# Kernel optimization log

Measured on AMD Instinct MI355X. Metric: run time of the kernel, lower is better.

Reference implementation:

```python
import jax, jax.numpy as jnp
import numpy as np
from jax import lax

GAMMA = 1.0  # init gamma


def setup_inputs() -> dict:
    key = jax.random.key(0)
    k = jax.random.split(key, 6)
    B, T1, T2, D, WD = 64, 320, 320, 768, 32
    x = jax.random.normal(k[0], (B, T1, D), jnp.float32)
    y = jax.random.normal(k[1], (B, T2, D), jnp.float32)
    # nn.Linear(input_dim, warp_dim): weight [WD, D], bias [WD]
    W = jax.random.normal(k[2], (WD, D), jnp.float32) / np.sqrt(D).astype(np.float32)
    b = 0.01 * jax.random.normal(k[3], (WD,), jnp.float32)
    warp_scale = 1.0 + 0.1 * jax.random.normal(k[4], (WD,), jnp.float32)
    warp_shift = 0.1 * jax.random.normal(k[5], (WD,), jnp.float32)
    return {"x": x, "y": y, "W": W, "b": b, "warp_scale": warp_scale, "warp_shift": warp_shift}


def _soft_dtw_path(xw, yw, gamma):
    # Faithful banded soft-DTW DP: cells outside the band stay 0 and ARE read
    # by in-band neighbors, exactly as the torch loop does.
    B, T1, _ = xw.shape
    T2 = yw.shape[1]
    bw = max(T1, T2) // 4 + 1
    # squared euclidean distances [B,T1,T2] (expanded form to avoid B*T1*T2*D blow-up)
    x2 = jnp.sum(xw * xw, -1)[:, :, None]
    y2 = jnp.sum(yw * yw, -1)[:, None, :]
    dist = x2 + y2 - 2.0 * jnp.einsum('bid,bjd->bij', xw, yw)
    NEG = jnp.float32(-1e30)  # disables a candidate inside logsumexp
    t2s = jnp.arange(T2)

    def outer(prev_row, xs):  # prev_row: path[t1-1, :] of shape [B,T2]
        t1, drow = xs  # drow: dist[:, t1, :] -> [B,T2]
        diag_prev = jnp.concatenate([jnp.zeros((B, 1), drow.dtype), prev_row[:, :-1]], axis=1)

        def inner(left, ins):  # left: path[t1, t2-1] -> [B]
            t2, d, up, diag = ins
            z = jnp.stack([
                jnp.where((t1 > 0) & (t2 > 0), -diag / gamma, NEG),
                jnp.where(t1 > 0, -up / gamma, NEG),
                jnp.where(t2 > 0, -left / gamma, NEG),
            ], axis=0)  # [3,B]
            softmin = -gamma * jax.nn.logsumexp(z, axis=0)
            val = d + jnp.where((t1 > 0) | (t2 > 0), softmin, 0.0)
            in_band = (t2 >= t1 - bw) & (t2 <= t1 + bw - 1)
            val = jnp.where(in_band, val, 0.0)
            return val, val

        _, row = lax.scan(inner, jnp.zeros((B,), drow.dtype),
                          (t2s, drow.T, prev_row.T, diag_prev.T))
        row = row.T  # [B,T2]
        return row, row

    _, path = lax.scan(outer, jnp.zeros((B, T2), dist.dtype),
                       (jnp.arange(T1), jnp.transpose(dist, (1, 0, 2))))
    path = jnp.transpose(path, (1, 0, 2))  # [B,T1,T2]
    return jax.nn.softmax(-path / gamma, axis=-1)


def reference(x, y, W, b, warp_scale, warp_shift):
    xw = (x @ W.T + b) * warp_scale + warp_shift
    yw = (y @ W.T + b) * warp_scale + warp_shift
    path = _soft_dtw_path(xw, yw, GAMMA)  # [B,T1,T2] softmax probs
    pn = path / (jnp.sum(path, axis=1, keepdims=True) + 1e-10)
    aligned = jnp.einsum('bts,btd->bsd', pn, x)  # bmm(path^T, x) -> [B,T2,D]
    return aligned, path
```

## Files before the change

### kernel.cpp

```cpp
#include <hip/hip_runtime.h>

#define NB 64
#define T 320
#define D 768
#define WD 32
#define NSTEP 639
#define NBLK 80
#define BSTRIDE (NBLK * 1024)
#define BIG 1e30f
#define LOG2E 1.44269504088896340736f
#define LN2 0.69314718055994530942f

__device__ __forceinline__ float dpp_ror1(float v) {
  return __int_as_float(__builtin_amdgcn_update_dpp(
      0, __float_as_int(v), 0x13C, 0xF, 0xF, true));
}
__device__ __forceinline__ float dpp_rol1(float v) {
  return __int_as_float(__builtin_amdgcn_update_dpp(
      0, __float_as_int(v), 0x134, 0xF, 0xF, true));
}

__global__ __launch_bounds__(256) void prep_kernel(
    const float* __restrict__ W, const float* __restrict__ bias,
    const float* __restrict__ wscale, const float* __restrict__ wshift,
    float* __restrict__ WeT, float* __restrict__ beff) {
  int i = blockIdx.x * 256 + threadIdx.x;
  int c = i >> 5, k = i & 31;
  WeT[i] = W[k * D + c] * wscale[k];
  if (i < WD) beff[i] = bias[i] * wscale[i] + wshift[i];
}

__global__ __launch_bounds__(256) void proj_kernel(
    const float* __restrict__ x, const float* __restrict__ y,
    const float* __restrict__ WeT, const float* __restrict__ beff,
    float* __restrict__ xw, float* __restrict__ yw) {
  __shared__ float lds[8448];
  int tid = threadIdx.x;
  int w = tid >> 6, l = tid & 63;
  int rbase = blockIdx.x * 64;
  float acc[32];
#pragma unroll
  for (int k = 0; k < 32; ++k) acc[k] = 0.f;
#pragma clang loop unroll(disable)
  for (int ch = 0; ch < 6; ++ch) {
    __syncthreads();
#pragma unroll
    for (int p = 0; p < 8; ++p) {
      int idx = p * 256 + tid;
      int row = idx >> 5;
      int c4 = idx & 31;
      int r = rbase + row;
      const float* src = (r < NB * T) ? x + (size_t)r * D
                                      : y + (size_t)(r - NB * T) * D;
      float4 v = *(const float4*)(src + ch * 128 + c4 * 4);
      lds[row * 129 + c4 * 4 + 0] = v.x;
      lds[row * 129 + c4 * 4 + 1] = v.y;
      lds[row * 129 + c4 * 4 + 2] = v.z;
      lds[row * 129 + c4 * 4 + 3] = v.w;
    }
    __syncthreads();
    int woff = __builtin_amdgcn_readfirstlane((ch * 128 + w * 32) * 32);
    const float* wp = WeT + woff;
#pragma unroll
    for (int cc = 0; cc < 32; ++cc) {
      float xv = lds[l * 129 + w * 32 + cc];
#pragma unroll
      for (int k = 0; k < 32; ++k)
        acc[k] = fmaf(wp[cc * 32 + k], xv, acc[k]);
    }
  }
  __syncthreads();
#pragma unroll
  for (int k = 0; k < 32; ++k) lds[w * 2112 + l * 33 + k] = acc[k];
  __syncthreads();
  int idx = tid * 8;
  int row = idx >> 5;
  int k0 = idx & 31;
  float o[8];
#pragma unroll
  for (int e = 0; e < 8; ++e)
    o[e] = lds[0 * 2112 + row * 33 + k0 + e] + lds[1 * 2112 + row * 33 + k0 + e] +
           lds[2 * 2112 + row * 33 + k0 + e] + lds[3 * 2112 + row * 33 + k0 + e] +
           beff[k0 + e];
  int rr = rbase + row;
  float* dst = (rr < NB * T) ? xw + (size_t)rr * WD + k0
                             : yw + (size_t)(rr - NB * T) * WD + k0;
  float4 o0 = {o[0], o[1], o[2], o[3]}, o1 = {o[4], o[5], o[6], o[7]};
  *(float4*)dst = o0;
  *(float4*)(dst + 4) = o1;
}

__global__ __launch_bounds__(256) void dist_kernel(
    const float* __restrict__ xw, const float* __restrict__ yw,
    float* __restrict__ dc) {
  __shared__ float xs[64][33];
  __shared__ float ys[64][33];
  int b = blockIdx.y;
  int cidx = blockIdx.x;
  int t1c = (cidx >> 2) * 64;
  int t2c = t1c - 88 + (cidx & 3) * 64;
  int tid = threadIdx.x;
  {
    int r = tid >> 2, c4 = tid & 3;
    const float* sx = xw + ((size_t)b * T + t1c + r) * WD;
    *(float4*)&xs[r][c4 * 4] = *(const float4*)(sx + c4 * 4);
    *(float4*)&xs[r][(c4 + 4) * 4] = *(const float4*)(sx + (c4 + 4) * 4);
    int t2r = t2c + r;
    if ((unsigned)t2r < (unsigned)T) {
      const float* sy = yw + ((size_t)b * T + t2r) * WD;
      *(float4*)&ys[r][c4 * 4] = *(const float4*)(sy + c4 * 4);
      *(float4*)&ys[r][(c4 + 4) * 4] = *(const float4*)(sy + (c4 + 4) * 4);
    }
  }
  __syncthreads();
  int ts1 = (tid >> 4) * 4;
  int ts2 = (tid & 15) * 4;
  float acc[4][4];
#pragma unroll
  for (int i = 0; i < 4; ++i)
#pragma unroll
    for (int j = 0; j < 4; ++j) acc[i][j] = 0.f;
#pragma unroll
  for (int c4 = 0; c4 < 8; ++c4) {
    float4 xv[4], yv[4];
#pragma unroll
    for (int i = 0; i < 4; ++i) xv[i] = *(const float4*)&xs[ts1 + i][c4 * 4];
#pragma unroll
    for (int j = 0; j < 4; ++j) yv[j] = *(const float4*)&ys[ts2 + j][c4 * 4];
#pragma unroll
    for (int i = 0; i < 4; ++i)
#pragma unroll
      for (int j = 0; j < 4; ++j) {
        float d0 = xv[i].x - yv[j].x, d1 = xv[i].y - yv[j].y;
        float d2 = xv[i].z - yv[j].z, d3 = xv[i].w - yv[j].w;
        float s = acc[i][j];
        s = fmaf(d0, d0, s); s = fmaf(d1, d1, s);
        s = fmaf(d2, d2, s); s = fmaf(d3, d3, s);
        acc[i][j] = s;
      }
  }
  float* dcb = dc + (size_t)b * BSTRIDE;
#pragma unroll
  for (int i = 0; i < 4; ++i) {
#pragma unroll
    for (int j = 0; j < 4; ++j) {
      int t1 = t1c + ts1 + i;
      int t2 = t2c + ts2 + j;
      int dt = t2 - t1;
      if ((unsigned)t2 < (unsigned)T && dt >= -81 && dt <= 80) {
        int d = t1 + t2;
        int par = (d + 1) & 1;
        int base = (d + 81 - par) >> 1;
        int a = base - t1;
        dcb[((d >> 3) << 10) + (a << 3) + (d & 7)] = acc[i][j] * LOG2E;
      }
    }
  }
}

#define FSTEP(DP_, DS_, PAR, DVAL)                                             \
  {                                                                            \
    const int d_ = (DVAL);                                                     \
    const int base_ = (d_ + 81 - (PAR)) >> 1;                                  \
    float shP, shS;                                                            \
    if (PAR) { shP = dpp_rol1((l == 0) ? v0b : v0); shS = dpp_rol1(v0b); }     \
    else     { shP = dpp_ror1(v1); shS = dpp_ror1((l == 63) ? v1 : v1b); }     \
    int t1 = base_ - l, t2 = d_ - t1;                                          \
    {                                                                          \
      bool valid = ((unsigned)t1 < (unsigned)T) && ((unsigned)t2 < (unsigned)T); \
      float up, left, diag;                                                    \
      if (PAR) { left = v0; up = shP; diag = v1; }                             \
      else     { up = v1; left = (l == 0) ? 0.f : shP; diag = v0; }            \
      float cu = (t1 > 0) ? up : BIG;                                          \
      float cl = (t2 > 0) ? left : BIG;                                        \
      float cd = (t1 > 0 && t2 > 0) ? diag : BIG;                              \
      float mn = fminf(fminf(cu, cl), cd);                                     \
      float mx = fmaxf(fmaxf(cu, cl), cd);                                     \
      float md = fmaxf(fminf(cu, cl), fminf(fmaxf(cu, cl), cd));               \
      float ss = 1.f + __builtin_amdgcn_exp2f(mn - md) +                       \
                 __builtin_amdgcn_exp2f(mn - mx);                              \
      float val = (DP_) + mn - __builtin_amdgcn_logf(ss);                      \
      if ((DVAL) == 0) val = (DP_);                                            \
      if (valid) {                                                             \
        if (PAR) v1 = val; else v0 = val;                                      \
        outb[t1 * T + t2] = val * LN2;                                         \
      }                                                                        \
    }                                                                          \
    {                                                                          \
      int t1b = t1 - 64, t2b = t2 + 64;                                        \
      bool valid = (l < 17) && ((unsigned)t1b < (unsigned)T) &&                \
                   ((unsigned)t2b < (unsigned)T);                              \
      float up, left, diag;                                                    \
      if (PAR) { left = v0b; up = (l == 16) ? 0.f : shS; diag = v1b; }         \
      else     { up = v1b; left = shS; diag = v0b; }                           \
      float cu = (t1b > 0) ? up : BIG;                                         \
      float cl = (t2b > 0) ? left : BIG;                                       \
      float cd = (t1b > 0 && t2b > 0) ? diag : BIG;                            \
      float mn = fminf(fminf(cu, cl), cd);                                     \
      float mx = fmaxf(fmaxf(cu, cl), cd);                                     \
      float md = fmaxf(fminf(cu, cl), fminf(fmaxf(cu, cl), cd));               \
      float ss = 1.f + __builtin_amdgcn_exp2f(mn - md) +                       \
                 __builtin_amdgcn_exp2f(mn - mx);                              \
      float val = (DS_) + mn - __builtin_amdgcn_logf(ss);                      \
      if (valid) {                                                             \
        if (PAR) v1b = val; else v0b = val;                                    \
        outb[t1b * T + t2b] = val * LN2;                                       \
      }                                                                        \
    }                                                                          \
  }

#define SSTEP(DP_, DS_, PAR, IOFF)                                             \
  {                                                                            \
    float shP, shS;                                                            \
    if (PAR) { shP = dpp_rol1((l == 0) ? v0b : v0); shS = dpp_rol1(v0b); }     \
    else     { shP = dpp_ror1(v1); shS = dpp_ror1((l == 63) ? v1 : v1b); }     \
    {                                                                          \
      float up, left, diag;                                                    \
      if (PAR) { left = v0; up = shP; diag = v1; }                             \
      else     { up = v1; left = (l == 0) ? 0.f : shP; diag = v0; }            \
      float mn = fminf(fminf(up, left), diag);                                 \
      float mx = fmaxf(fmaxf(up, left), diag);                                 \
      float md = fmaxf(fminf(up, left), fminf(fmaxf(up, left), diag));         \
      float ss = 1.f + __builtin_amdgcn_exp2f(mn - md) +                       \
                 __builtin_amdgcn_exp2f(mn - mx);                              \
      float val = (DP_) + mn - __builtin_amdgcn_logf(ss);                      \
      if (PAR) v1 = val; else v0 = val;                                        \
      outb[io + (IOFF)] = val * LN2;                                           \
    }                                                                          \
    {                                                                          \
      float up, left, diag;                                                    \
      if (PAR) { left = v0b; up = (l == 16) ? 0.f : shS; diag = v1b; }         \
      else     { up = v1b; left = shS; diag = v0b; }                           \
      float mn = fminf(fminf(up, left), diag);                                 \
      float mx = fmaxf(fmaxf(up, left), diag);                                 \
      float md = fmaxf(fminf(up, left), fminf(fmaxf(up, left), diag));         \
      float ss = 1.f + __builtin_amdgcn_exp2f(mn - md) +                       \
                 __builtin_amdgcn_exp2f(mn - mx);                              \
      float val = (DS_) + mn - __builtin_amdgcn_logf(ss);                      \
      if (PAR) v1b = val; else v0b = val;                                      \
      if (l < 17) outb[ioS + (IOFF)] = val * LN2;                              \
    }                                                                          \
  }

#define LOADBLK(R0, R1, S0v, S1v, DBLK)                                        \
  {                                                                            \
    const float4* q_ = (const float4*)(dcb + (DBLK) * 1024 + l * 8);           \
    R0 = q_[0]; R1 = q_[1];                                                    \
    const float4* q2_ = (const float4*)(dcb + (DBLK) * 1024 + (64 + l) * 8);   \
    S0v = q2_[0]; S1v = q2_[1];                                                \
  }

#define BLK8_F(P0, P1, S0v, S1v, DB)                                           \
  FSTEP(P0.x, S0v.x, 1, (DB) + 0) FSTEP(P0.y, S0v.y, 0, (DB) + 1)              \
  FSTEP(P0.z, S0v.z, 1, (DB) + 2) FSTEP(P0.w, S0v.w, 0, (DB) + 3)              \
  FSTEP(P1.x, S1v.x, 1, (DB) + 4) FSTEP(P1.y, S1v.y, 0, (DB) + 5)              \
  FSTEP(P1.z, S1v.z, 1, (DB) + 6) FSTEP(P1.w, S1v.w, 0, (DB) + 7)

#define BLK8_S(P0, P1, S0v, S1v)                                               \
  SSTEP(P0.x, S0v.x, 1, 0)   SSTEP(P0.y, S0v.y, 0, 320)                        \
  SSTEP(P0.z, S0v.z, 1, 321) SSTEP(P0.w, S0v.w, 0, 641)                        \
  io += 642; ioS += 642;                                                       \
  SSTEP(P1.x, S1v.x, 1, 0)   SSTEP(P1.y, S1v.y, 0, 320)                        \
  SSTEP(P1.z, S1v.z, 1, 321) SSTEP(P1.w, S1v.w, 0, 641)                        \
  io += 642; ioS += 642;

__global__ __launch_bounds__(64) void dtw_kernel(
    const float* __restrict__ dc, float* __restrict__ path) {
  int b = blockIdx.x;
  int l = threadIdx.x;
  const float* dcb = dc + (size_t)b * BSTRIDE;
  float* outb = path + (size_t)b * T * T;
  float v0 = 0.f, v1 = 0.f, v0b = 0.f, v1b = 0.f;
  float4 aP0, aP1, aS0, aS1, bP0, bP1, bS0, bS1;
  int io = 0, ioS = 0;

  if (l == 40) {
    float d00 = dcb[320];
    v1 = d00;
    outb[0] = d00 * LN2;
  }
  LOADBLK(aP0, aP1, aS0, aS1, 0)
#pragma clang loop unroll(disable)
  for (int it = 0; it < 6; ++it) {
    int dbase = it * 16;
    int blk = it * 2;
    LOADBLK(bP0, bP1, bS0, bS1, blk + 1)
    BLK8_F(aP0, aP1, aS0, aS1, dbase)
    LOADBLK(aP0, aP1, aS0, aS1, blk + 2)
    BLK8_F(bP0, bP1, bS0, bS1, dbase + 8)
  }
  io = 28168 - 319 * l;
  ioS = io - 20416;
#pragma clang loop unroll(disable)
  for (int it = 0; it < 27; ++it) {
    int blk = 12 + it * 2;
    LOADBLK(bP0, bP1, bS0, bS1, blk + 1)
    BLK8_S(aP0, aP1, aS0, aS1)
    LOADBLK(aP0, aP1, aS0, aS1, blk + 2)
    BLK8_S(bP0, bP1, bS0, bS1)
  }
#pragma clang loop unroll(disable)
  for (int it = 0; it < 6; ++it) {
    int dbase = 528 + it * 16;
    int blk = 66 + it * 2;
    LOADBLK(bP0, bP1, bS0, bS1, blk + 1)
    BLK8_F(aP0, aP1, aS0, aS1, dbase)
    LOADBLK(aP0, aP1, aS0, aS1, blk + 2)
    BLK8_F(bP0, bP1, bS0, bS1, dbase + 8)
  }
  LOADBLK(bP0, bP1, bS0, bS1, 79)
  BLK8_F(aP0, aP1, aS0, aS1, 624)
  FSTEP(bP0.x, bS0.x, 1, 632) FSTEP(bP0.y, bS0.y, 0, 633)
  FSTEP(bP0.z, bS0.z, 1, 634) FSTEP(bP0.w, bS0.w, 0, 635)
  FSTEP(bP1.x, bS1.x, 1, 636) FSTEP(bP1.y, bS1.y, 0, 637)
  FSTEP(bP1.z, bS1.z, 1, 638)
}

__global__ __launch_bounds__(T) void softmax_kernel(float* __restrict__ path,
                                                    float* __restrict__ cvec) {
  __shared__ float sm1[5], sm2[5];
  int row = blockIdx.x;
  int t1 = row % T;
  int j = threadIdx.x;
  float* p = path + (size_t)row * T;
  bool in = (j >= t1 - 81) && (j <= t1 + 80);
  float v = in ? p[j] : 0.f;
  float m = v;
#pragma unroll
  for (int off = 32; off >= 1; off >>= 1) m = fminf(m, __shfl_xor(m, off, 64));
  int w = j >> 6;
  if ((j & 63) == 0) sm1[w] = m;
  __syncthreads();
  m = fminf(fminf(fminf(sm1[0], sm1[1]), fminf(sm1[2], sm1[3])), sm1[4]);
  float e = __expf(m - v);
  float s = e;
#pragma unroll
  for (int off = 32; off >= 1; off >>= 1) s += __shfl_xor(s, off, 64);
  if ((j & 63) == 0) sm2[w] = s;
  __syncthreads();
  s = sm2[0] + sm2[1] + sm2[2] + sm2[3] + sm2[4];
  p[j] = e / s;
  if (j == 0) cvec[row] = __expf(m - 0.f) / s;
}

__global__ __launch_bounds__(256) void gk_kernel(
    const float* __restrict__ x, const float* __restrict__ cvec,
    float* __restrict__ g) {
  int b = blockIdx.y;
  int d0 = blockIdx.x * 256 + threadIdx.x;
  const float* xb = x + (size_t)b * T * D + d0;
  const float* cb = cvec + b * T;
  float s = 0.f;
  for (int t = 0; t < T; ++t) s = fmaf(cb[t], xb[(size_t)t * D], s);
  g[b * D + d0] = s;
}

__global__ __launch_bounds__(256) void colsum_kernel(
    const float* __restrict__ path, const float* __restrict__ cvec,
    float* __restrict__ scale) {
  __shared__ float red[4][64];
  __shared__ float cbred[4];
  int b = blockIdx.y;
  int tid = threadIdx.x;
  int l = tid & 63, tq = tid >> 6;
  int j = blockIdx.x * 64 + l;
  const float* cb = cvec + b * T;
  float c = cb[tid];
  if (tid < 64) c += cb[256 + tid];
#pragma unroll
  for (int off = 32; off >= 1; off >>= 1) c += __shfl_xor(c, off, 64);
  if (l == 0) cbred[tq] = c;
  float s = 0.f;
  int t0 = j - 80 + tq * 41;
  const float* p = path + (size_t)b * T * T + j;
#pragma unroll 4
  for (int i = 0; i < 41; ++i) {
    int t = t0 + i;
    if ((unsigned)t < (unsigned)T) s += p[(size_t)t * T] - cb[t];
  }
  red[tq][l] = s;
  __syncthreads();
  if (tq == 0) {
    float cs = red[0][l] + red[1][l] + red[2][l] + red[3][l] +
               (cbred[0] + cbred[1] + cbred[2] + cbred[3]);
    scale[b * T + j] = 1.f / (cs + 1e-10f);
  }
}

#define TSB 64
#define TDB 128
#define TKB 16
__global__ __launch_bounds__(256) void bmm_kernel(
    const float* __restrict__ path, const float* __restrict__ x,
    const float* __restrict__ cvec, const float* __restrict__ g,
    const float* __restrict__ scale, float* __restrict__ out) {
  __shared__ __align__(16) float Pl[TKB][TSB];
  __shared__ __align__(16) float Xl[TKB][TDB];
  int bid = blockIdx.x;
  int wgid = (bid & 7) * 240 + (bid >> 3);
  int b = wgid / 30;
  int r = wgid - b * 30;
  int s0 = (r / 6) * TSB;
  int d0 = (r % 6) * TDB;
  int tid = threadIdx.x;
  int ts = tid & 15, td = tid >> 4;
  const float* pb = path + (size_t)b * T * T;
  const float* xb = x + (size_t)b * T * D;
  const float* cb = cvec + b * T;
  float acc[4][8];
  {
    const float* gb = g + b * D + d0 + td * 8;
    float4 g0 = *(const float4*)gb;
    float4 g1 = *(const float4*)(gb + 4);
    float gv[8] = {g0.x, g0.y, g0.z, g0.w, g1.x, g1.y, g1.z, g1.w};
#pragma unroll
    for (int i = 0; i < 4; ++i)
#pragma unroll
      for (int jj = 0; jj < 8; ++jj) acc[i][jj] = gv[jj];
  }
  int t_lo = s0 - 80; if (t_lo < 0) t_lo = 0; t_lo &= ~15;
  int t_hi = (s0 + 160) & ~15; if (t_hi > T) t_hi = T;
  for (int t0 = t_lo; t0 < t_hi; t0 += TKB) {
    __syncthreads();
    {
      int tr = tid >> 4, sc = (tid & 15) * 4;
      float4 p4 = *(const float4*)&pb[(size_t)(t0 + tr) * T + s0 + sc];
      float cv = cb[t0 + tr];
      p4.x -= cv; p4.y -= cv; p4.z -= cv; p4.w -= cv;
      *(float4*)&Pl[tr][sc] = p4;
    }
    {
      int tr = tid >> 4, c0 = (tid & 15) * 4;
      const float* xrow = &xb[(size_t)(t0 + tr) * D + d0 + c0];
      *(float4*)&Xl[tr][c0] = *(const float4*)(xrow);
      *(float4*)&Xl[tr][c0 + 64] = *(const float4*)(xrow + 64);
    }
    __syncthreads();
#pragma unroll
    for (int t = 0; t < TKB; ++t) {
      float4 pa = *(const float4*)&Pl[t][ts * 4];
      float4 xa = *(const float4*)&Xl[t][td * 8];
      float4 xc = *(const float4*)&Xl[t][td * 8 + 4];
      float pv[4] = {pa.x, pa.y, pa.z, pa.w};
      float xv[8] = {xa.x, xa.y, xa.z, xa.w, xc.x, xc.y, xc.z, xc.w};
#pragma unroll
      for (int i = 0; i < 4; ++i)
#pragma unroll
        for (int jj = 0; jj < 8; ++jj)
          acc[i][jj] = fmaf(pv[i], xv[jj], acc[i][jj]);
    }
  }
#pragma unroll
  for (int i = 0; i < 4; ++i) {
    int s = s0 + ts * 4 + i;
    float sc = scale[b * T + s];
    float* op = out + ((size_t)b * T + s) * D + d0 + td * 8;
    float4 o0, o1;
    o0.x = acc[i][0] * sc; o0.y = acc[i][1] * sc; o0.z = acc[i][2] * sc; o0.w = acc[i][3] * sc;
    o1.x = acc[i][4] * sc; o1.y = acc[i][5] * sc; o1.z = acc[i][6] * sc; o1.w = acc[i][7] * sc;
    *(float4*)op = o0;
    *(float4*)(op + 4) = o1;
  }
}

extern "C" void kernel_launch(void* const* d_in, const int* in_sizes, int n_in,
                              void* d_out, int out_size, void* d_ws, size_t ws_size,
                              hipStream_t stream) {
  const float* x = (const float*)d_in[0];
  const float* y = (const float*)d_in[1];
  const float* W = (const float*)d_in[2];
  const float* bias = (const float*)d_in[3];
  const float* wscale = (const float*)d_in[4];
  const float* wshift = (const float*)d_in[5];
  float* outp = (float*)d_out;
  float* aligned = outp;
  float* path = outp + (size_t)NB * T * D;
  float* distc = aligned;
  float* ws = (float*)d_ws;
  float* xw = ws;
  float* yw = xw + (size_t)NB * T * WD;
  float* scale = yw + (size_t)NB * T * WD;
  float* WeT = scale + (size_t)NB * T;
  float* beff = WeT + (size_t)WD * D;
  float* cvec = beff + WD;
  float* g = cvec + (size_t)NB * T;

  prep_kernel<<<dim3((WD * D) / 256), 256, 0, stream>>>(W, bias, wscale, wshift, WeT, beff);
  proj_kernel<<<dim3((2 * NB * T) / 64), 256, 0, stream>>>(x, y, WeT, beff, xw, yw);
  dist_kernel<<<dim3(20, NB), 256, 0, stream>>>(xw, yw, distc);
  dtw_kernel<<<dim3(NB), 64, 0, stream>>>(distc, path);
  softmax_kernel<<<dim3(NB * T), T, 0, stream>>>(path, cvec);
  gk_kernel<<<dim3(D / 256, NB), 256, 0, stream>>>(x, cvec, g);
  colsum_kernel<<<dim3(T / 64, NB), 256, 0, stream>>>(path, cvec, scale);
  bmm_kernel<<<dim3((D / TDB) * (T / TSB) * NB), 256, 0, stream>>>(path, x, cvec, g, scale, aligned);
}
```

Measured before the change: 325.8 us.

## Interleave two batch DTW recurrences per wavefront and keep path in log2 domain

The DTW wavefront kernel now processes two batch items per 64-lane block. It runs their anti-diagonal recurrences interleaved, so the two independent dependency chains can hide each other's exp/log and DPP latency, and the grid is halved. The path is stored in log2 units without the LN2 rescale, and softmax switches to exp2 to match. This saves a multiply per cell, but doubles register use and per-wave instruction count, so the serial critical path per wave may grow if latency is not the bottleneck.

```diff
diff --git a/kernel.cpp b/kernel.cpp
--- a/kernel.cpp
+++ b/kernel.cpp
@@ -9,7 +9,6 @@
 #define BSTRIDE (NBLK * 1024)
 #define BIG 1e30f
 #define LOG2E 1.44269504088896340736f
-#define LN2 0.69314718055994530942f
 
 __device__ __forceinline__ float dpp_ror1(float v) {
   return __int_as_float(__builtin_amdgcn_update_dpp(
@@ -158,19 +157,19 @@
   }
 }
 
-#define FSTEP(DP_, DS_, PAR, DVAL)                                             \
+#define FSTEPN(N, DP_, DS_, PAR, DVAL)                                         \
   {                                                                            \
     const int d_ = (DVAL);                                                     \
     const int base_ = (d_ + 81 - (PAR)) >> 1;                                  \
     float shP, shS;                                                            \
-    if (PAR) { shP = dpp_rol1((l == 0) ? v0b : v0); shS = dpp_rol1(v0b); }     \
-    else     { shP = dpp_ror1(v1); shS = dpp_ror1((l == 63) ? v1 : v1b); }     \
+    if (PAR) { shP = dpp_rol1((l == 0) ? v0b_##N : v0_##N); shS = dpp_rol1(v0b_##N); } \
+    else     { shP = dpp_ror1(v1_##N); shS = dpp_ror1((l == 63) ? v1_##N : v1b_##N); } \
     int t1 = base_ - l, t2 = d_ - t1;                                          \
     {                                                                          \
       bool valid = ((unsigned)t1 < (unsigned)T) && ((unsigned)t2 < (unsigned)T); \
       float up, left, diag;                                                    \
-      if (PAR) { left = v0; up = shP; diag = v1; }                             \
-      else     { up = v1; left = (l == 0) ? 0.f : shP; diag = v0; }            \
+      if (PAR) { left = v0_##N; up = shP; diag = v1_##N; }                     \
+      else     { up = v1_##N; left = (l == 0) ? 0.f : shP; diag = v0_##N; }    \
       float cu = (t1 > 0) ? up : BIG;                                          \
       float cl = (t2 > 0) ? left : BIG;                                        \
       float cd = (t1 > 0 && t2 > 0) ? diag : BIG;                              \
@@ -182,8 +181,8 @@
       float val = (DP_) + mn - __builtin_amdgcn_logf(ss);                      \
       if ((DVAL) == 0) val = (DP_);                                            \
       if (valid) {                                                             \
-        if (PAR) v1 = val; else v0 = val;                                      \
-        outb[t1 * T + t2] = val * LN2;                                         \
+        if (PAR) v1_##N = val; else v0_##N = val;                              \
+        outb_##N[t1 * T + t2] = val;                                           \
       }                                                                        \
     }                                                                          \
     {                                                                          \
@@ -191,8 +190,8 @@
       bool valid = (l < 17) && ((unsigned)t1b < (unsigned)T) &&                \
                    ((unsigned)t2b < (unsigned)T);                              \
       float up, left, diag;                                                    \
-      if (PAR) { left = v0b; up = (l == 16) ? 0.f : shS; diag = v1b; }         \
-      else     { up = v1b; left = shS; diag = v0b; }                           \
+      if (PAR) { left = v0b_##N; up = (l == 16) ? 0.f : shS; diag = v1b_##N; } \
+      else     { up = v1b_##N; left = shS; diag = v0b_##N; }                   \
       float cu = (t1b > 0) ? up : BIG;                                         \
       float cl = (t2b > 0) ? left : BIG;                                       \
       float cd = (t1b > 0 && t2b > 0) ? diag : BIG;                            \
@@ -203,117 +202,131 @@
                  __builtin_amdgcn_exp2f(mn - mx);                              \
       float val = (DS_) + mn - __builtin_amdgcn_logf(ss);                      \
       if (valid) {                                                             \
-        if (PAR) v1b = val; else v0b = val;                                    \
-        outb[t1b * T + t2b] = val * LN2;                                       \
+        if (PAR) v1b_##N = val; else v0b_##N = val;                            \
+        outb_##N[t1b * T + t2b] = val;                                         \
       }                                                                        \
     }                                                                          \
   }
 
-#define SSTEP(DP_, DS_, PAR, IOFF)                                             \
+#define SSTEPN(N, DP_, DS_, PAR, IOFF)                                         \
   {                                                                            \
     float shP, shS;                                                            \
-    if (PAR) { shP = dpp_rol1((l == 0) ? v0b : v0); shS = dpp_rol1(v0b); }     \
-    else     { shP = dpp_ror1(v1); shS = dpp_ror1((l == 63) ? v1 : v1b); }     \
+    if (PAR) { shP = dpp_rol1((l == 0) ? v0b_##N : v0_##N); shS = dpp_rol1(v0b_##N); } \
+    else     { shP = dpp_ror1(v1_##N); shS = dpp_ror1((l == 63) ? v1_##N : v1b_##N); } \
     {                                                                          \
       float up, left, diag;                                                    \
-      if (PAR) { left = v0; up = shP; diag = v1; }                             \
-      else     { up = v1; left = (l == 0) ? 0.f : shP; diag = v0; }            \
+      if (PAR) { left = v0_##N; up = shP; diag = v1_##N; }                     \
+      else     { up = v1_##N; left = (l == 0) ? 0.f : shP; diag = v0_##N; }    \
       float mn = fminf(fminf(up, left), diag);                                 \
       float mx = fmaxf(fmaxf(up, left), diag);                                 \
       float md = fmaxf(fminf(up, left), fminf(fmaxf(up, left), diag));         \
       float ss = 1.f + __builtin_amdgcn_exp2f(mn - md) +                       \
                  __builtin_amdgcn_exp2f(mn - mx);                              \
       float val = (DP_) + mn - __builtin_amdgcn_logf(ss);                      \
-      if (PAR) v1 = val; else v0 = val;                                        \
-      outb[io + (IOFF)] = val * LN2;                                           \
+      if (PAR) v1_##N = val; else v0_##N = val;                                \
+      outb_##N[io_##N + (IOFF)] = val;                                         \
     }                                                                          \
     {                                                                          \
       float up, left, diag;                                                    \
-      if (PAR) { left = v0b; up = (l == 16) ? 0.f : shS; diag = v1b; }         \
-      else     { up = v1b; left = shS; diag = v0b; }                           \
+      if (PAR) { left = v0b_##N; up = (l == 16) ? 0.f : shS; diag = v1b_##N; } \
+      else     { up = v1b_##N; left = shS; diag = v0b_##N; }                   \
       float mn = fminf(fminf(up, left), diag);                                 \
       float mx = fmaxf(fmaxf(up, left), diag);                                 \
       float md = fmaxf(fminf(up, left), fminf(fmaxf(up, left), diag));         \
       float ss = 1.f + __builtin_amdgcn_exp2f(mn - md) +                       \
                  __builtin_amdgcn_exp2f(mn - mx);                              \
       float val = (DS_) + mn - __builtin_amdgcn_logf(ss);                      \
-      if (PAR) v1b = val; else v0b = val;                                      \
-      if (l < 17) outb[ioS + (IOFF)] = val * LN2;                              \
+      if (PAR) v1b_##N = val; else v0b_##N = val;                              \
+      if (l < 17) outb_##N[ioS_##N + (IOFF)] = val;                            \
     }                                                                          \
   }
 
-#define LOADBLK(R0, R1, S0v, S1v, DBLK)                                        \
+#define LOADBLK2(Q, DBLK)                                                      \
   {                                                                            \
-    const float4* q_ = (const float4*)(dcb + (DBLK) * 1024 + l * 8);           \
-    R0 = q_[0]; R1 = q_[1];                                                    \
-    const float4* q2_ = (const float4*)(dcb + (DBLK) * 1024 + (64 + l) * 8);   \
-    S0v = q2_[0]; S1v = q2_[1];                                                \
-  }
-
-#define BLK8_F(P0, P1, S0v, S1v, DB)                                           \
-  FSTEP(P0.x, S0v.x, 1, (DB) + 0) FSTEP(P0.y, S0v.y, 0, (DB) + 1)              \
-  FSTEP(P0.z, S0v.z, 1, (DB) + 2) FSTEP(P0.w, S0v.w, 0, (DB) + 3)              \
-  FSTEP(P1.x, S1v.x, 1, (DB) + 4) FSTEP(P1.y, S1v.y, 0, (DB) + 5)              \
-  FSTEP(P1.z, S1v.z, 1, (DB) + 6) FSTEP(P1.w, S1v.w, 0, (DB) + 7)
-
-#define BLK8_S(P0, P1, S0v, S1v)                                               \
-  SSTEP(P0.x, S0v.x, 1, 0)   SSTEP(P0.y, S0v.y, 0, 320)                        \
-  SSTEP(P0.z, S0v.z, 1, 321) SSTEP(P0.w, S0v.w, 0, 641)                        \
-  io += 642; ioS += 642;                                                       \
-  SSTEP(P1.x, S1v.x, 1, 0)   SSTEP(P1.y, S1v.y, 0, 320)                        \
-  SSTEP(P1.z, S1v.z, 1, 321) SSTEP(P1.w, S1v.w, 0, 641)                        \
-  io += 642; ioS += 642;
-
-__global__ __launch_bounds__(64) void dtw_kernel(
+    const float4* q0 = (const float4*)(dcb_0 + (DBLK) * 1024 + l * 8);         \
+    Q##P0_0 = q0[0]; Q##P1_0 = q0[1];                                          \
+    const float4* q0s = (const float4*)(dcb_0 + (DBLK) * 1024 + (64 + l) * 8); \
+    Q##S0_0 = q0s[0]; Q##S1_0 = q0s[1];                                        \
+    const float4* q1 = (const float4*)(dcb_1 + (DBLK) * 1024 + l * 8);         \
+    Q##P0_1 = q1[0]; Q##P1_1 = q1[1];                                          \
+    const float4* q1s = (const float4*)(dcb_1 + (DBLK) * 1024 + (64 + l) * 8); \
+    Q##S0_1 = q1s[0]; Q##S1_1 = q1s[1];                                        \
+  }
+
+#define BLK8_F2(Q, DB)                                                                       \
+  FSTEPN(0, Q##P0_0.x, Q##S0_0.x, 1, (DB) + 0) FSTEPN(1, Q##P0_1.x, Q##S0_1.x, 1, (DB) + 0) \
+  FSTEPN(0, Q##P0_0.y, Q##S0_0.y, 0, (DB) + 1) FSTEPN(1, Q##P0_1.y, Q##S0_1.y, 0, (DB) + 1) \
+  FSTEPN(0, Q##P0_0.z, Q##S0_0.z, 1, (DB) + 2) FSTEPN(1, Q##P0_1.z, Q##S0_1.z, 1, (DB) + 2) \
+  FSTEPN(0, Q##P0_0.w, Q##S0_0.w, 0, (DB) + 3) FSTEPN(1, Q##P0_1.w, Q##S0_1.w, 0, (DB) + 3) \
+  FSTEPN(0, Q##P1_0.x, Q##S1_0.x, 1, (DB) + 4) FSTEPN(1, Q##P1_1.x, Q##S1_1.x, 1, (DB) + 4) \
+  FSTEPN(0, Q##P1_0.y, Q##S1_0.y, 0, (DB) + 5) FSTEPN(1, Q##P1_1.y, Q##S1_1.y, 0, (DB) + 5) \
+  FSTEPN(0, Q##P1_0.z, Q##S1_0.z, 1, (DB) + 6) FSTEPN(1, Q##P1_1.z, Q##S1_1.z, 1, (DB) + 6) \
+  FSTEPN(0, Q##P1_0.w, Q##S1_0.w, 0, (DB) + 7) FSTEPN(1, Q##P1_1.w, Q##S1_1.w, 0, (DB) + 7)
+
+#define BLK8_S2(Q)                                                                 \
+  SSTEPN(0, Q##P0_0.x, Q##S0_0.x, 1, 0)   SSTEPN(1, Q##P0_1.x, Q##S0_1.x, 1, 0)   \
+  SSTEPN(0, Q##P0_0.y, Q##S0_0.y, 0, 320) SSTEPN(1, Q##P0_1.y, Q##S0_1.y, 0, 320) \
+  SSTEPN(0, Q##P0_0.z, Q##S0_0.z, 1, 321) SSTEPN(1, Q##P0_1.z, Q##S0_1.z, 1, 321) \
+  SSTEPN(0, Q##P0_0.w, Q##S0_0.w, 0, 641) SSTEPN(1, Q##P0_1.w, Q##S0_1.w, 0, 641) \
+  io_0 += 642; ioS_0 += 642; io_1 += 642; ioS_1 += 642;                            \
+  SSTEPN(0, Q##P1_0.x, Q##S1_0.x, 1, 0)   SSTEPN(1, Q##P1_1.x, Q##S1_1.x, 1, 0)   \
+  SSTEPN(0, Q##P1_0.y, Q##S1_0.y, 0, 320) SSTEPN(1, Q##P1_1.y, Q##S1_1.y, 0, 320) \
+  SSTEPN(0, Q##P1_0.z, Q##S1_0.z, 1, 321) SSTEPN(1, Q##P1_1.z, Q##S1_1.z, 1, 321) \
+  SSTEPN(0, Q##P1_0.w, Q##S1_0.w, 0, 641) SSTEPN(1, Q##P1_1.w, Q##S1_1.w, 0, 641) \
+  io_0 += 642; ioS_0 += 642; io_1 += 642; ioS_1 += 642;
+
+__global__ __launch_bounds__(64, 1) void dtw_kernel(
     const float* __restrict__ dc, float* __restrict__ path) {
-  int b = blockIdx.x;
+  int bq = blockIdx.x;
   int l = threadIdx.x;
-  const float* dcb = dc + (size_t)b * BSTRIDE;
-  float* outb = path + (size_t)b * T * T;
-  float v0 = 0.f, v1 = 0.f, v0b = 0.f, v1b = 0.f;
-  float4 aP0, aP1, aS0, aS1, bP0, bP1, bS0, bS1;
-  int io = 0, ioS = 0;
-
-  if (l == 40) {
-    float d00 = dcb[320];
-    v1 = d00;
-    outb[0] = d00 * LN2;
-  }
-  LOADBLK(aP0, aP1, aS0, aS1, 0)
+  const float* dcb_0 = dc + (size_t)(2 * bq) * BSTRIDE;
+  const float* dcb_1 = dc + (size_t)(2 * bq + 1) * BSTRIDE;
+  float* outb_0 = path + (size_t)(2 * bq) * T * T;
+  float* outb_1 = path + (size_t)(2 * bq + 1) * T * T;
+  float v0_0 = 0.f, v1_0 = 0.f, v0b_0 = 0.f, v1b_0 = 0.f;
+  float v0_1 = 0.f, v1_1 = 0.f, v0b_1 = 0.f, v1b_1 = 0.f;
+  float4 aP0_0, aP1_0, aS0_0, aS1_0, bP0_0, bP1_0, bS0_0, bS1_0;
+  float4 aP0_1, aP1_1, aS0_1, aS1_1, bP0_1, bP1_1, bS0_1, bS1_1;
+  int io_0 = 0, ioS_0 = 0, io_1 = 0, ioS_1 = 0;
+
+  LOADBLK2(a, 0)
 #pragma clang loop unroll(disable)
   for (int it = 0; it < 6; ++it) {
     int dbase = it * 16;
     int blk = it * 2;
-    LOADBLK(bP0, bP1, bS0, bS1, blk + 1)
-    BLK8_F(aP0, aP1, aS0, aS1, dbase)
-    LOADBLK(aP0, aP1, aS0, aS1, blk + 2)
-    BLK8_F(bP0, bP1, bS0, bS1, dbase + 8)
-  }
-  io = 28168 - 319 * l;
-  ioS = io - 20416;
+    LOADBLK2(b, blk + 1)
+    BLK8_F2(a, dbase)
+    LOADBLK2(a, blk + 2)
+    BLK8_F2(b, dbase + 8)
+  }
+  io_0 = 28168 - 319 * l; ioS_0 = io_0 - 20416;
+  io_1 = 28168 - 319 * l; ioS_1 = io_1 - 20416;
 #pragma clang loop unroll(disable)
   for (int it = 0; it < 27; ++it) {
     int blk = 12 + it * 2;
-    LOADBLK(bP0, bP1, bS0, bS1, blk + 1)
-    BLK8_S(aP0, aP1, aS0, aS1)
-    LOADBLK(aP0, aP1, aS0, aS1, blk + 2)
-    BLK8_S(bP0, bP1, bS0, bS1)
+    LOADBLK2(b, blk + 1)
+    BLK8_S2(a)
+    LOADBLK2(a, blk + 2)
+    BLK8_S2(b)
   }
 #pragma clang loop unroll(disable)
   for (int it = 0; it < 6; ++it) {
     int dbase = 528 + it * 16;
     int blk = 66 + it * 2;
-    LOADBLK(bP0, bP1, bS0, bS1, blk + 1)
-    BLK8_F(aP0, aP1, aS0, aS1, dbase)
-    LOADBLK(aP0, aP1, aS0, aS1, blk + 2)
-    BLK8_F(bP0, bP1, bS0, bS1, dbase + 8)
-  }
-  LOADBLK(bP0, bP1, bS0, bS1, 79)
-  BLK8_F(aP0, aP1, aS0, aS1, 624)
-  FSTEP(bP0.x, bS0.x, 1, 632) FSTEP(bP0.y, bS0.y, 0, 633)
-  FSTEP(bP0.z, bS0.z, 1, 634) FSTEP(bP0.w, bS0.w, 0, 635)
-  FSTEP(bP1.x, bS1.x, 1, 636) FSTEP(bP1.y, bS1.y, 0, 637)
-  FSTEP(bP1.z, bS1.z, 1, 638)
+    LOADBLK2(b, blk + 1)
+    BLK8_F2(a, dbase)
+    LOADBLK2(a, blk + 2)
+    BLK8_F2(b, dbase + 8)
+  }
+  LOADBLK2(b, 79)
+  BLK8_F2(a, 624)
+  FSTEPN(0, bP0_0.x, bS0_0.x, 1, 632) FSTEPN(1, bP0_1.x, bS0_1.x, 1, 632)
+  FSTEPN(0, bP0_0.y, bS0_0.y, 0, 633) FSTEPN(1, bP0_1.y, bS0_1.y, 0, 633)
+  FSTEPN(0, bP0_0.z, bS0_0.z, 1, 634) FSTEPN(1, bP0_1.z, bS0_1.z, 1, 634)
+  FSTEPN(0, bP0_0.w, bS0_0.w, 0, 635) FSTEPN(1, bP0_1.w, bS0_1.w, 0, 635)
+  FSTEPN(0, bP1_0.x, bS1_0.x, 1, 636) FSTEPN(1, bP1_1.x, bS1_1.x, 1, 636)
+  FSTEPN(0, bP1_0.y, bS1_0.y, 0, 637) FSTEPN(1, bP1_1.y, bS1_1.y, 0, 637)
+  FSTEPN(0, bP1_0.z, bS1_0.z, 1, 638) FSTEPN(1, bP1_1.z, bS1_1.z, 1, 638)
 }
 
 __global__ __launch_bounds__(T) void softmax_kernel(float* __restrict__ path,
@@ -332,7 +345,7 @@
   if ((j & 63) == 0) sm1[w] = m;
   __syncthreads();
   m = fminf(fminf(fminf(sm1[0], sm1[1]), fminf(sm1[2], sm1[3])), sm1[4]);
-  float e = __expf(m - v);
+  float e = __builtin_amdgcn_exp2f(m - v);
   float s = e;
 #pragma unroll
   for (int off = 32; off >= 1; off >>= 1) s += __shfl_xor(s, off, 64);
@@ -340,7 +353,7 @@
   __syncthreads();
   s = sm2[0] + sm2[1] + sm2[2] + sm2[3] + sm2[4];
   p[j] = e / s;
-  if (j == 0) cvec[row] = __expf(m - 0.f) / s;
+  if (j == 0) cvec[row] = __builtin_amdgcn_exp2f(m - 0.f) / s;
 }
 
 __global__ __launch_bounds__(256) void gk_kernel(
@@ -488,7 +501,7 @@
   prep_kernel<<<dim3((WD * D) / 256), 256, 0, stream>>>(W, bias, wscale, wshift, WeT, beff);
   proj_kernel<<<dim3((2 * NB * T) / 64), 256, 0, stream>>>(x, y, WeT, beff, xw, yw);
   dist_kernel<<<dim3(20, NB), 256, 0, stream>>>(xw, yw, distc);
-  dtw_kernel<<<dim3(NB), 64, 0, stream>>>(distc, path);
+  dtw_kernel<<<dim3(NB / 2), 64, 0, stream>>>(distc, path);
   softmax_kernel<<<dim3(NB * T), T, 0, stream>>>(path, cvec);
   gk_kernel<<<dim3(D / 256, NB), 256, 0, stream>>>(x, cvec, g);
   colsum_kernel<<<dim3(T / 64, NB), 256, 0, stream>>>(path, cvec, scale);
```

After: 393.5 us. 20.7% more time.
